# Performance work log

Measured on AMD Instinct MI355X. Metric: run time of the kernel, lower is better.

The kernel has to match this reference:

```python
import jax, jax.numpy as jnp
import numpy as np

MARGIN = 0.0


def setup_inputs() -> dict:
    key = jax.random.key(0)
    k1, k2, k3 = jax.random.split(key, 3)
    n, d = 8192, 128
    inputs = jax.random.normal(k1, (n, d), dtype=jnp.float32)
    targets = jax.random.randint(k2, (n,), 0, 512, dtype=jnp.int64)
    cids = jax.random.randint(k3, (n,), 0, 8, dtype=jnp.int64)
    return {"inputs": inputs, "targets": targets, "cids": cids}


def _margin_ranking_loss(x1, x2, margin):
    # nn.MarginRankingLoss with y=1: mean(max(0, -(x1 - x2) + margin))
    return jnp.mean(jnp.maximum(x2 - x1 + margin, 0.0))


def reference(inputs, targets, cids):
    n = inputs.shape[0]
    # pairwise euclidean distance matrix [n, n]
    sq = jnp.sum(inputs * inputs, axis=1)              # [n]
    d2 = sq[:, None] + sq[None, :] - 2.0 * (inputs @ inputs.T)
    dist = jnp.sqrt(jnp.clip(d2, 1e-12, 1e12))         # [n, n]

    mask = targets[:, None] == targets[None, :]        # [n, n] same-identity
    # view_mask (cids) is computed in the original but never used

    # hardest positive (max over same-id, incl. self) and hardest negative (min over diff-id)
    pos_masked = jnp.where(mask, dist, -jnp.inf)
    neg_masked = jnp.where(mask, jnp.inf, dist)
    dist_ap = jnp.max(pos_masked, axis=1)              # [n]
    dist_an = jnp.min(neg_masked, axis=1)              # [n]
    p2_ind = jnp.argmax(pos_masked, axis=1)            # [n]
    n1_ind = jnp.argmin(neg_masked, axis=1)            # [n]

    # secondary neighbors: hardest-negative of the hardest negative,
    # hardest-positive of the hardest positive (row lookups)
    dist_n12 = dist_an[n1_ind]                         # min of dist[n1_ind] over ~mask[n1_ind]
    dist_p12 = dist_ap[p2_ind]                         # max of dist[p2_ind] over mask[p2_ind]

    loss = (_margin_ranking_loss(dist_an, dist_ap, MARGIN)
            + 0.1 * _margin_ranking_loss(dist_n12, dist_ap, MARGIN)
            + 0.1 * _margin_ranking_loss(dist_an, dist_p12, MARGIN))
    prec = jnp.mean((dist_an > dist_ap).astype(jnp.float32))
    return loss, prec, dist
```

## Files before the change

### kernel.cpp

```cpp
#include <hip/hip_runtime.h>

#define NROWS 8192
#define DDIM 128

typedef unsigned short u16;
typedef unsigned int u32;
typedef unsigned long long u64;
typedef __attribute__((ext_vector_type(4))) float f32x4;
typedef __attribute__((ext_vector_type(2))) float f32x2;
typedef __attribute__((ext_vector_type(4))) int i32x4;
typedef __attribute__((ext_vector_type(8))) short short8;

__device__ __forceinline__ u16 f32_to_bf16(float f){
  u32 u = __float_as_uint(f);
  u32 r = (u + 0x7FFFu + ((u >> 16) & 1u)) >> 16;
  return (u16)r;
}
__device__ __forceinline__ float bf16_to_f32(u16 h){ return __uint_as_float(((u32)h) << 16); }

__global__ __launch_bounds__(256) void pack_kernel(const float* __restrict__ in,
                                                   u16* __restrict__ phi, u16* __restrict__ plo,
                                                   float* __restrict__ sq,
                                                   u64* __restrict__ pos_key, u64* __restrict__ neg_key){
  int t = blockIdx.x * 256 + threadIdx.x;
  if (t < NROWS){ pos_key[t] = 0ull; neg_key[t] = 0xFFFFFFFFFFFFFFFFull; }
  int r = t >> 4, s = t & 15;
  const float* src = in + (size_t)r * DDIM + s * 8;
  f32x4 a = *(const f32x4*)(src);
  f32x4 b = *(const f32x4*)(src + 4);
  float x[8] = {a.x, a.y, a.z, a.w, b.x, b.y, b.z, b.w};
  short8 hv, lv;
  float ss = 0.f;
  #pragma unroll
  for (int j = 0; j < 8; ++j){
    u16 h = f32_to_bf16(x[j]);
    u16 l = f32_to_bf16(x[j] - bf16_to_f32(h));
    hv[j] = (short)h; lv[j] = (short)l;
    ss += x[j] * x[j];
  }
  size_t dst = (((size_t)(r >> 4) * 4 + (s >> 2)) * 64 + (s & 3) * 16 + (r & 15)) * 8;
  *(short8*)(phi + dst) = hv;
  *(short8*)(plo + dst) = lv;
  #pragma unroll
  for (int m = 1; m < 16; m <<= 1) ss += __shfl_xor(ss, m, 64);
  if (s == 0) sq[r] = ss;
}

__global__ __launch_bounds__(256, 2) void dist_kernel(
    const u16* __restrict__ phi, const u16* __restrict__ plo,
    const float* __restrict__ sq, const int* __restrict__ tgt,
    float* __restrict__ dist, u64* __restrict__ pos_key, u64* __restrict__ neg_key)
{
  int id = blockIdx.x;
  int xcd = id & 7, r9 = id >> 3;
  int cx = xcd >> 1, cy = xcd & 1;
  const int bi = cx * 16 + (r9 >> 5);
  const int bj = cy * 32 + (r9 & 31);

  const int tid = threadIdx.x;
  const int w = tid >> 6, lane = tid & 63;
  const int wr = w >> 1, wc = w & 1;
  const int lr = lane & 15, g = lane >> 4;

  f32x4 acc[4][4] = {};

  short8 bufA[2][8], bufB[2][8];
  #pragma unroll
  for (int m = 0; m < 4; ++m){
    size_t offA = ((size_t)(((bi * 8 + wr * 4 + m) * 4 + 0) * 64) + lane) * 8;
    bufA[0][m * 2 + 0] = *(const short8*)(phi + offA);
    bufA[0][m * 2 + 1] = *(const short8*)(plo + offA);
    size_t offB = ((size_t)(((bj * 8 + wc * 4 + m) * 4 + 0) * 64) + lane) * 8;
    bufB[0][m * 2 + 0] = *(const short8*)(phi + offB);
    bufB[0][m * 2 + 1] = *(const short8*)(plo + offB);
  }
  #pragma unroll
  for (int kk = 0; kk < 4; ++kk){
    const int cur = kk & 1, nxt = cur ^ 1;
    if (kk < 3){
      #pragma unroll
      for (int m = 0; m < 4; ++m){
        size_t offA = ((size_t)(((bi * 8 + wr * 4 + m) * 4 + (kk + 1)) * 64) + lane) * 8;
        bufA[nxt][m * 2 + 0] = *(const short8*)(phi + offA);
        bufA[nxt][m * 2 + 1] = *(const short8*)(plo + offA);
        size_t offB = ((size_t)(((bj * 8 + wc * 4 + m) * 4 + (kk + 1)) * 64) + lane) * 8;
        bufB[nxt][m * 2 + 0] = *(const short8*)(phi + offB);
        bufB[nxt][m * 2 + 1] = *(const short8*)(plo + offB);
      }
    }
    #pragma unroll
    for (int m = 0; m < 4; ++m)
      #pragma unroll
      for (int n = 0; n < 4; ++n){
        acc[m][n] = __builtin_amdgcn_mfma_f32_16x16x32_bf16(bufB[cur][n*2+0], bufA[cur][m*2+0], acc[m][n], 0, 0, 0);
        acc[m][n] = __builtin_amdgcn_mfma_f32_16x16x32_bf16(bufB[cur][n*2+1], bufA[cur][m*2+0], acc[m][n], 0, 0, 0);
        acc[m][n] = __builtin_amdgcn_mfma_f32_16x16x32_bf16(bufB[cur][n*2+0], bufA[cur][m*2+1], acc[m][n], 0, 0, 0);
      }
  }

  f32x4 sqc[4]; i32x4 tcv[4]; int cbase[4];
  #pragma unroll
  for (int n = 0; n < 4; ++n){
    cbase[n] = bj * 128 + wc * 64 + n * 16 + g * 4;
    sqc[n] = *(const f32x4*)(sq + cbase[n]);
    tcv[n] = *(const i32x4*)(tgt + cbase[n]);
  }
  #pragma unroll
  for (int m = 0; m < 4; ++m){
    const int grow = bi * 128 + wr * 64 + m * 16 + lr;
    const float sqr = sq[grow];
    const int tr = tgt[grow];
    float bpv = -1.f, bnv = 3.0e38f; int bpc = 0x7FFFFFFF, bnc = 0x7FFFFFFF;
    float* drow = dist + (size_t)grow * NROWS;
    #pragma unroll
    for (int n = 0; n < 4; ++n){
      f32x4 dd4;
      #pragma unroll
      for (int r = 0; r < 4; ++r){
        float d2 = sqr + sqc[n][r] - 2.f * acc[m][n][r];
        d2 = fminf(fmaxf(d2, 1e-12f), 1e12f);
        dd4[r] = sqrtf(d2);
        if (tr == tcv[n][r]){
          if (d2 > bpv){ bpv = d2; bpc = cbase[n] + r; }
        } else {
          if (d2 < bnv){ bnv = d2; bnc = cbase[n] + r; }
        }
      }
      *(f32x2*)(drow + cbase[n])     = f32x2{dd4.x, dd4.y};
      *(f32x2*)(drow + cbase[n] + 2) = f32x2{dd4.z, dd4.w};
    }
    #pragma unroll
    for (int msk = 16; msk <= 32; msk <<= 1){
      float ov = __shfl_xor(bpv, msk, 64); int oc = __shfl_xor(bpc, msk, 64);
      if (ov > bpv || (ov == bpv && oc < bpc)){ bpv = ov; bpc = oc; }
      ov = __shfl_xor(bnv, msk, 64); oc = __shfl_xor(bnc, msk, 64);
      if (ov < bnv || (ov == bnv && oc < bnc)){ bnv = ov; bnc = oc; }
    }
    if (g == 0){
      if (bpv >= 0.f)
        atomicMax(&pos_key[grow],
                  ((u64)__float_as_uint(sqrtf(bpv)) << 32) | (u64)(0xFFFFFFFFu - (u32)bpc));
      if (bnv < 3.0e38f)
        atomicMin(&neg_key[grow],
                  ((u64)__float_as_uint(sqrtf(bnv)) << 32) | (u64)(u32)bnc);
    }
  }
}

__global__ __launch_bounds__(256) void decode_kernel(const u64* __restrict__ pk, const u64* __restrict__ nk,
                                                     float* __restrict__ ap, float* __restrict__ an,
                                                     int* __restrict__ p2, int* __restrict__ n1){
  int i = blockIdx.x * 256 + threadIdx.x;
  u64 p = pk[i], q = nk[i];
  ap[i] = __uint_as_float((u32)(p >> 32));
  p2[i] = (int)(0xFFFFFFFFu - (u32)(p & 0xFFFFFFFFu));
  an[i] = __uint_as_float((u32)(q >> 32));
  n1[i] = (int)(u32)(q & 0xFFFFFFFFu);
}

__global__ __launch_bounds__(1024) void final_kernel(const float* __restrict__ ap, const float* __restrict__ an,
                                                     const int* __restrict__ p2, const int* __restrict__ n1,
                                                     float* __restrict__ out){
  __shared__ float r1[1024], r2[1024], r3[1024]; __shared__ int r4[1024];
  int tid = threadIdx.x;
  float s1 = 0.f, s2 = 0.f, s3 = 0.f; int pc = 0;
  for (int i = tid; i < NROWS; i += 1024){
    float a = ap[i], b = an[i];
    float n12 = an[n1[i]];
    float p12 = ap[p2[i]];
    s1 += fmaxf(a - b, 0.f);
    s2 += fmaxf(a - n12, 0.f);
    s3 += fmaxf(p12 - b, 0.f);
    pc += (b > a) ? 1 : 0;
  }
  r1[tid] = s1; r2[tid] = s2; r3[tid] = s3; r4[tid] = pc;
  __syncthreads();
  for (int s = 512; s > 0; s >>= 1){
    if (tid < s){ r1[tid] += r1[tid + s]; r2[tid] += r2[tid + s]; r3[tid] += r3[tid + s]; r4[tid] += r4[tid + s]; }
    __syncthreads();
  }
  if (tid == 0){
    float inv = 1.f / (float)NROWS;
    out[0] = r1[0] * inv + 0.1f * (r2[0] * inv) + 0.1f * (r3[0] * inv);
    out[1] = (float)r4[0] * inv;
  }
}

extern "C" void kernel_launch(void* const* d_in, const int* in_sizes, int n_in,
                              void* d_out, int out_size, void* d_ws, size_t ws_size,
                              hipStream_t stream){
  const float* inputs = (const float*)d_in[0];
  const int* targets = (const int*)d_in[1];
  float* out = (float*)d_out;
  char* ws = (char*)d_ws;

  u16* phi = (u16*)ws;
  u16* plo = (u16*)(ws + (2u << 20));
  float* sq = (float*)(ws + (4u << 20));
  u64* pos_key = (u64*)(ws + (4u << 20) + (64u << 10));
  u64* neg_key = (u64*)(ws + (4u << 20) + (128u << 10));
  float* ap = (float*)(ws + (4u << 20) + (192u << 10));
  float* an = (float*)(ws + (4u << 20) + (224u << 10));
  int* p2 = (int*)(ws + (4u << 20) + (256u << 10));
  int* n1 = (int*)(ws + (4u << 20) + (288u << 10));

  pack_kernel<<<(NROWS * 16) / 256, 256, 0, stream>>>(inputs, phi, plo, sq, pos_key, neg_key);
  dist_kernel<<<64 * 64, 256, 0, stream>>>(phi, plo, sq, targets, out + 2, pos_key, neg_key);
  decode_kernel<<<NROWS / 256, 256, 0, stream>>>(pos_key, neg_key, ap, an, p2, n1);
  final_kernel<<<1, 1024, 0, stream>>>(ap, an, p2, n1, out);
}
```

Baseline: 150.7 us.

## Fuse decode into final reduction, use fast sqrt and wider dist stores

Removes the separate decode kernel: the final single-block kernel now unpacks the packed max/min keys itself into shared memory and does the gathered lookups from LDS. The distance epilogue switches to the hardware sqrt builtin and replaces two 8-byte stores with one 16-byte store of reduced alignment. This saves one kernel launch and a global round trip, and trims epilogue instructions. The precision count becomes a float accumulation, and the hardware sqrt may differ slightly from the correctly rounded version.

```diff
diff --git a/kernel.cpp b/kernel.cpp
--- a/kernel.cpp
+++ b/kernel.cpp
@@ -7,6 +7,7 @@
 typedef unsigned int u32;
 typedef unsigned long long u64;
 typedef __attribute__((ext_vector_type(4))) float f32x4;
+typedef __attribute__((ext_vector_type(4), aligned(8))) float f32x4u;
 typedef __attribute__((ext_vector_type(2))) float f32x2;
 typedef __attribute__((ext_vector_type(4))) int i32x4;
 typedef __attribute__((ext_vector_type(8))) short short8;
@@ -119,15 +120,14 @@
       for (int r = 0; r < 4; ++r){
         float d2 = sqr + sqc[n][r] - 2.f * acc[m][n][r];
         d2 = fminf(fmaxf(d2, 1e-12f), 1e12f);
-        dd4[r] = sqrtf(d2);
+        dd4[r] = __builtin_amdgcn_sqrtf(d2);
         if (tr == tcv[n][r]){
           if (d2 > bpv){ bpv = d2; bpc = cbase[n] + r; }
         } else {
           if (d2 < bnv){ bnv = d2; bnc = cbase[n] + r; }
         }
       }
-      *(f32x2*)(drow + cbase[n])     = f32x2{dd4.x, dd4.y};
-      *(f32x2*)(drow + cbase[n] + 2) = f32x2{dd4.z, dd4.w};
+      *(f32x4u*)(drow + cbase[n]) = dd4;
     }
     #pragma unroll
     for (int msk = 16; msk <= 32; msk <<= 1){
@@ -139,40 +139,44 @@
     if (g == 0){
       if (bpv >= 0.f)
         atomicMax(&pos_key[grow],
-                  ((u64)__float_as_uint(sqrtf(bpv)) << 32) | (u64)(0xFFFFFFFFu - (u32)bpc));
+                  ((u64)__float_as_uint(__builtin_amdgcn_sqrtf(bpv)) << 32) | (u64)(0xFFFFFFFFu - (u32)bpc));
       if (bnv < 3.0e38f)
         atomicMin(&neg_key[grow],
-                  ((u64)__float_as_uint(sqrtf(bnv)) << 32) | (u64)(u32)bnc);
-    }
-  }
-}
-
-__global__ __launch_bounds__(256) void decode_kernel(const u64* __restrict__ pk, const u64* __restrict__ nk,
-                                                     float* __restrict__ ap, float* __restrict__ an,
-                                                     int* __restrict__ p2, int* __restrict__ n1){
-  int i = blockIdx.x * 256 + threadIdx.x;
-  u64 p = pk[i], q = nk[i];
-  ap[i] = __uint_as_float((u32)(p >> 32));
-  p2[i] = (int)(0xFFFFFFFFu - (u32)(p & 0xFFFFFFFFu));
-  an[i] = __uint_as_float((u32)(q >> 32));
-  n1[i] = (int)(u32)(q & 0xFFFFFFFFu);
-}
-
-__global__ __launch_bounds__(1024) void final_kernel(const float* __restrict__ ap, const float* __restrict__ an,
-                                                     const int* __restrict__ p2, const int* __restrict__ n1,
+                  ((u64)__float_as_uint(__builtin_amdgcn_sqrtf(bnv)) << 32) | (u64)(u32)bnc);
+    }
+  }
+}
+
+__global__ __launch_bounds__(1024) void final_kernel(const u64* __restrict__ pk, const u64* __restrict__ nk,
                                                      float* __restrict__ out){
-  __shared__ float r1[1024], r2[1024], r3[1024]; __shared__ int r4[1024];
+  __shared__ float s_ap[NROWS];
+  __shared__ float s_an[NROWS];
   int tid = threadIdx.x;
-  float s1 = 0.f, s2 = 0.f, s3 = 0.f; int pc = 0;
-  for (int i = tid; i < NROWS; i += 1024){
-    float a = ap[i], b = an[i];
-    float n12 = an[n1[i]];
-    float p12 = ap[p2[i]];
+  int p2r[8], n1r[8];
+  #pragma unroll
+  for (int j = 0; j < 8; ++j){
+    int i = tid + j * 1024;
+    u64 p = pk[i], q = nk[i];
+    s_ap[i] = __uint_as_float((u32)(p >> 32));
+    s_an[i] = __uint_as_float((u32)(q >> 32));
+    p2r[j] = (int)(0xFFFFFFFFu - (u32)(p & 0xFFFFFFFFu));
+    n1r[j] = (int)(u32)(q & 0xFFFFFFFFu);
+  }
+  __syncthreads();
+  float s1 = 0.f, s2 = 0.f, s3 = 0.f; float pc = 0.f;
+  #pragma unroll
+  for (int j = 0; j < 8; ++j){
+    int i = tid + j * 1024;
+    float a = s_ap[i], b = s_an[i];
+    float n12 = s_an[n1r[j]];
+    float p12 = s_ap[p2r[j]];
     s1 += fmaxf(a - b, 0.f);
     s2 += fmaxf(a - n12, 0.f);
     s3 += fmaxf(p12 - b, 0.f);
-    pc += (b > a) ? 1 : 0;
-  }
+    pc += (b > a) ? 1.f : 0.f;
+  }
+  __syncthreads();
+  float* r1 = s_ap; float* r2 = s_ap + 1024; float* r3 = s_an; float* r4 = s_an + 1024;
   r1[tid] = s1; r2[tid] = s2; r3[tid] = s3; r4[tid] = pc;
   __syncthreads();
   for (int s = 512; s > 0; s >>= 1){
@@ -182,7 +186,7 @@
   if (tid == 0){
     float inv = 1.f / (float)NROWS;
     out[0] = r1[0] * inv + 0.1f * (r2[0] * inv) + 0.1f * (r3[0] * inv);
-    out[1] = (float)r4[0] * inv;
+    out[1] = r4[0] * inv;
   }
 }
 
@@ -199,13 +203,8 @@
   float* sq = (float*)(ws + (4u << 20));
   u64* pos_key = (u64*)(ws + (4u << 20) + (64u << 10));
   u64* neg_key = (u64*)(ws + (4u << 20) + (128u << 10));
-  float* ap = (float*)(ws + (4u << 20) + (192u << 10));
-  float* an = (float*)(ws + (4u << 20) + (224u << 10));
-  int* p2 = (int*)(ws + (4u << 20) + (256u << 10));
-  int* n1 = (int*)(ws + (4u << 20) + (288u << 10));
 
   pack_kernel<<<(NROWS * 16) / 256, 256, 0, stream>>>(inputs, phi, plo, sq, pos_key, neg_key);
   dist_kernel<<<64 * 64, 256, 0, stream>>>(phi, plo, sq, targets, out + 2, pos_key, neg_key);
-  decode_kernel<<<NROWS / 256, 256, 0, stream>>>(pos_key, neg_key, ap, an, p2, n1);
-  final_kernel<<<1, 1024, 0, stream>>>(ap, an, p2, n1, out);
-}
+  final_kernel<<<1, 1024, 0, stream>>>(pos_key, neg_key, out);
+}
```

Result: faster. 128.1 us (-15.0%).
